# Kernel tuning notes

Hardware: AMD Instinct MI355X
Metric: run time of the kernel (lower is better)

The kernel has to match this reference:

```python
import jax, jax.numpy as jnp
import numpy as np

K = 3
LAST_DIM = 128
IM_H, IM_W = 1024.0, 1536.0
CROP = 2 * K  # tf.image.crop_and_resize crop size [2k, 2k]


def crop_and_resize(image, boxes, box_ids, crop_size):
    """Faithful port of tf.image.crop_and_resize (bilinear, extrapolation=0).
    image: (B,H,W,C); boxes: (N,4) normalized [y1,x1,y2,x2]; box_ids: (N,) int32.
    Returns (N, S, S, C)."""
    H, W = image.shape[1], image.shape[2]
    S = crop_size
    y1, x1, y2, x2 = boxes[:, 0], boxes[:, 1], boxes[:, 2], boxes[:, 3]
    s = jnp.arange(S, dtype=boxes.dtype)
    # sampling coordinates (S > 1 branch of TF)
    ys = y1[:, None] * (H - 1) + s[None, :] * ((y2 - y1)[:, None] * (H - 1) / (S - 1))  # (N,S)
    xs = x1[:, None] * (W - 1) + s[None, :] * ((x2 - x1)[:, None] * (W - 1) / (S - 1))  # (N,S)
    valid_y = (ys >= 0) & (ys <= H - 1)
    valid_x = (xs >= 0) & (xs <= W - 1)
    y0f = jnp.floor(ys)
    x0f = jnp.floor(xs)
    ly = ys - y0f  # bilinear fractions
    lx = xs - x0f
    y0i = jnp.clip(y0f.astype(jnp.int32), 0, H - 1)
    y1i = jnp.clip(y0i + 1, 0, H - 1)
    x0i = jnp.clip(x0f.astype(jnp.int32), 0, W - 1)
    x1i = jnp.clip(x0i + 1, 0, W - 1)
    b = box_ids[:, None, None]

    def g(yi, xi):
        # gather (N,S,S,C) corner values
        return image[b, yi[:, :, None], xi[:, None, :]]

    lx_b = lx[:, None, :, None]
    top = g(y0i, x0i) * (1 - lx_b) + g(y0i, x1i) * lx_b
    bot = g(y1i, x0i) * (1 - lx_b) + g(y1i, x1i) * lx_b
    ly_b = ly[:, :, None, None]
    out = top * (1 - ly_b) + bot * ly_b
    mask = (valid_y[:, :, None] & valid_x[:, None, :]).astype(out.dtype)[..., None]
    return out * mask


def setup_inputs() -> dict:
    key = jax.random.key(0)
    k_feat, k_bid, k_xy, k_wh = jax.random.split(key, 4)
    B, H, W = 4, 64, 96
    N = 2048
    feature_maps = jax.random.normal(k_feat, (B, H, W, K * K * LAST_DIM), dtype=jnp.float32)
    batch_ids = jax.random.randint(k_bid, (N,), 0, B).astype(jnp.float32)
    # top-left corners in image coords, plausible box sizes
    xy = jax.random.uniform(k_xy, (N, 2), dtype=jnp.float32)
    wh = jax.random.uniform(k_wh, (N, 2), dtype=jnp.float32)
    x1 = xy[:, 0] * (0.7 * IM_W)
    y1 = xy[:, 1] * (0.7 * IM_H)
    x2 = x1 + 32.0 + wh[:, 0] * (0.3 * IM_W - 32.0)
    y2 = y1 + 32.0 + wh[:, 1] * (0.3 * IM_H - 32.0)
    rois = jnp.stack([batch_ids, x1, y1, x2, y2], axis=-1)
    return {"feature_maps": feature_maps, "rois": rois}


def reference(feature_maps, rois):
    k = K
    rois = rois.reshape(-1, 5)
    batch_ids = rois[:, 0].astype(jnp.int32)
    norm = jnp.array([IM_W, IM_H, IM_W, IM_H], dtype=rois.dtype)
    bx = rois[:, 1:] / norm                                   # x1,y1,x2,y2 normalized
    boxes = jnp.stack([bx[:, 1], bx[:, 0], bx[:, 3], bx[:, 2]], axis=-1)  # y1,x1,y2,x2
    bin_w = (boxes[:, 3] - boxes[:, 1]) / k
    bin_h = boxes[:, 2] - boxes[:, 0] / k  # faithful bug: missing parens in original
    C = feature_maps.shape[-1] // (k * k)
    acc = 0.0
    for ih in range(k):
        for iw in range(k):
            idx = ih * k + iw
            # faithful bug: fourth coordinate uses bin_h instead of bin_w
            box = jnp.stack([
                boxes[:, 0] + ih * bin_h,
                boxes[:, 1] + iw * bin_w,
                boxes[:, 0] + (ih + 1) * bin_h,
                boxes[:, 1] + (iw + 1) * bin_h,
            ], axis=-1)
            feat = feature_maps[..., idx * C:(idx + 1) * C]
            acc = acc + crop_and_resize(feat, box, batch_ids, CROP)
    sensitive = acc / (k * k)           # (N, 2k, 2k, C)
    out = jnp.mean(sensitive, axis=(1, 2))  # (N, C)
    return out[None]                    # (1, N, C)
```

## Files before the change

kernel.cpp:

```cpp
#include <hip/hip_runtime.h>

constexpr int   CC      = 128;
constexpr int   WSTRIDE = 9 * 128;
constexpr int   HSTRIDE = 96 * WSTRIDE;
constexpr long  BSTRIDE = 64L * HSTRIDE;

__global__ __launch_bounds__(576)
void rroi_pool_kernel(const float* __restrict__ feat,
                      const float* __restrict__ rois,
                      float* __restrict__ out, int N) {
  const int n = blockIdx.x;
  const int wid  = threadIdx.x >> 6;
  const int lane = threadIdx.x & 63;

  __shared__ float partial[9][CC];

  const float r0  = rois[n * 5 + 0];
  const float rx1 = rois[n * 5 + 1];
  const float ry1 = rois[n * 5 + 2];
  const float rx2 = rois[n * 5 + 3];
  const float ry2 = rois[n * 5 + 4];
  const int b = (int)r0;

  const float x1 = rx1 / 1536.0f;
  const float y1 = ry1 / 1024.0f;
  const float x2 = rx2 / 1536.0f;
  const float y2 = ry2 / 1024.0f;

  const float bin_w = (x2 - x1) / 3.0f;
  const float bin_h = y2 - y1 / 3.0f;

  const int ih = wid / 3;
  const int iw = wid - 3 * ih;

  const float by1 = y1 + (float)ih * bin_h;
  const float bx1 = x1 + (float)iw * bin_w;
  const float by2 = y1 + (float)(ih + 1) * bin_h;
  const float bx2 = x1 + (float)(iw + 1) * bin_h;

  const float ystep = ((by2 - by1) * 63.0f) / 5.0f;
  const float xstep = ((bx2 - bx1) * 95.0f) / 5.0f;
  const float ybase = by1 * 63.0f;
  const float xbase = bx1 * 95.0f;

  int   xo0[6], xo1[6];
  float lx[6];
  bool  vx[6];
#pragma unroll
  for (int sx = 0; sx < 6; ++sx) {
    const float xs = xbase + (float)sx * xstep;
    vx[sx] = (xs >= 0.0f) && (xs <= 95.0f);
    const float xf = floorf(xs);
    lx[sx] = xs - xf;
    int xi = (int)xf;
    xi = xi < 0 ? 0 : (xi > 95 ? 95 : xi);
    const int xj = (xi + 1 > 95) ? 95 : xi + 1;
    xo0[sx] = xi * WSTRIDE;
    xo1[sx] = xj * WSTRIDE;
  }

  float acc0 = 0.0f, acc1 = 0.0f;
  const float* fb = feat + (size_t)b * BSTRIDE + wid * CC + 2 * lane;

#pragma unroll
  for (int sy = 0; sy < 6; ++sy) {
    const float ys = ybase + (float)sy * ystep;
    if (!((ys >= 0.0f) && (ys <= 63.0f))) continue;
    const float yf = floorf(ys);
    const float ly = ys - yf;
    int yi = (int)yf;
    yi = yi < 0 ? 0 : (yi > 63 ? 63 : yi);
    const int yj = (yi + 1 > 63) ? 63 : yi + 1;
    const float* row0 = fb + (size_t)yi * HSTRIDE;
    const float* row1 = fb + (size_t)yj * HSTRIDE;
#pragma unroll
    for (int sx = 0; sx < 6; ++sx) {
      if (!vx[sx]) continue;
      const float l = lx[sx];
      const float2 v00 = *(const float2*)(row0 + xo0[sx]);
      const float2 v01 = *(const float2*)(row0 + xo1[sx]);
      const float2 v10 = *(const float2*)(row1 + xo0[sx]);
      const float2 v11 = *(const float2*)(row1 + xo1[sx]);
      const float t0 = v00.x * (1.0f - l) + v01.x * l;
      const float t1 = v00.y * (1.0f - l) + v01.y * l;
      const float u0 = v10.x * (1.0f - l) + v11.x * l;
      const float u1 = v10.y * (1.0f - l) + v11.y * l;
      acc0 += t0 * (1.0f - ly) + u0 * ly;
      acc1 += t1 * (1.0f - ly) + u1 * ly;
    }
  }

  partial[wid][2 * lane]     = acc0;
  partial[wid][2 * lane + 1] = acc1;
  __syncthreads();

  if (threadIdx.x < CC) {
    const float scale = 1.0f / 324.0f;
    float s = 0.0f;
#pragma unroll
    for (int w = 0; w < 9; ++w) s += partial[w][threadIdx.x];
    out[(size_t)n * CC + threadIdx.x] = s * scale;
  }
}

extern "C" void kernel_launch(void* const* d_in, const int* in_sizes, int n_in,
                              void* d_out, int out_size, void* d_ws, size_t ws_size,
                              hipStream_t stream) {
  const float* feat = (const float*)d_in[0];
  const float* rois = (const float*)d_in[1];
  float* out = (float*)d_out;
  const int N = in_sizes[1] / 5;
  rroi_pool_kernel<<<N, 576, 0, stream>>>(feat, rois, out, N);
}
```

Before: 97.99 us.

## Split pooling into per-subbox wave kernel plus separate reduction kernel

```diff
diff --git a/kernel.cpp b/kernel.cpp
--- a/kernel.cpp
+++ b/kernel.cpp
@@ -5,16 +5,10 @@
 constexpr int   HSTRIDE = 96 * WSTRIDE;
 constexpr long  BSTRIDE = 64L * HSTRIDE;
 
-__global__ __launch_bounds__(576)
-void rroi_pool_kernel(const float* __restrict__ feat,
-                      const float* __restrict__ rois,
-                      float* __restrict__ out, int N) {
-  const int n = blockIdx.x;
-  const int wid  = threadIdx.x >> 6;
-  const int lane = threadIdx.x & 63;
-
-  __shared__ float partial[9][CC];
-
+__device__ __forceinline__ void subbox_accum(const float* __restrict__ feat,
+                                             const float* __restrict__ rois,
+                                             int n, int wid, int lane,
+                                             float& acc0, float& acc1) {
   const float r0  = rois[n * 5 + 0];
   const float rx1 = rois[n * 5 + 1];
   const float ry1 = rois[n * 5 + 2];
@@ -59,7 +53,6 @@
     xo1[sx] = xj * WSTRIDE;
   }
 
-  float acc0 = 0.0f, acc1 = 0.0f;
   const float* fb = feat + (size_t)b * BSTRIDE + wid * CC + 2 * lane;
 
 #pragma unroll
@@ -89,17 +82,57 @@
       acc1 += t1 * (1.0f - ly) + u1 * ly;
     }
   }
+}
+
+__global__ __launch_bounds__(64)
+void rroi_partial_kernel(const float* __restrict__ feat,
+                         const float* __restrict__ rois,
+                         float* __restrict__ ws) {
+  const int wid  = blockIdx.x;
+  const int n    = blockIdx.y;
+  const int lane = threadIdx.x;
+
+  float acc0 = 0.0f, acc1 = 0.0f;
+  subbox_accum(feat, rois, n, wid, lane, acc0, acc1);
+
+  float* p = ws + ((size_t)n * 9 + wid) * CC;
+  p[2 * lane]     = acc0;
+  p[2 * lane + 1] = acc1;
+}
+
+__global__ __launch_bounds__(128)
+void rroi_reduce_kernel(const float* __restrict__ ws,
+                        float* __restrict__ out) {
+  const int n = blockIdx.x;
+  const int c = threadIdx.x;
+  const float* p = ws + (size_t)n * 9 * CC + c;
+  float s = 0.0f;
+#pragma unroll
+  for (int w = 0; w < 9; ++w) s += p[w * CC];
+  out[(size_t)n * CC + c] = s * (1.0f / 324.0f);
+}
+
+__global__ __launch_bounds__(576)
+void rroi_pool_kernel(const float* __restrict__ feat,
+                      const float* __restrict__ rois,
+                      float* __restrict__ out, int N) {
+  const int n = blockIdx.x;
+  const int wid  = threadIdx.x >> 6;
+  const int lane = threadIdx.x & 63;
+  __shared__ float partial[9][CC];
+
+  float acc0 = 0.0f, acc1 = 0.0f;
+  subbox_accum(feat, rois, n, wid, lane, acc0, acc1);
 
   partial[wid][2 * lane]     = acc0;
   partial[wid][2 * lane + 1] = acc1;
   __syncthreads();
 
   if (threadIdx.x < CC) {
-    const float scale = 1.0f / 324.0f;
     float s = 0.0f;
 #pragma unroll
     for (int w = 0; w < 9; ++w) s += partial[w][threadIdx.x];
-    out[(size_t)n * CC + threadIdx.x] = s * scale;
+    out[(size_t)n * CC + threadIdx.x] = s * (1.0f / 324.0f);
   }
 }
 
@@ -110,5 +143,14 @@
   const float* rois = (const float*)d_in[1];
   float* out = (float*)d_out;
   const int N = in_sizes[1] / 5;
-  rroi_pool_kernel<<<N, 576, 0, stream>>>(feat, rois, out, N);
+
+  const size_t need = (size_t)N * 9 * CC * sizeof(float);
+  if (ws_size >= need) {
+    float* ws = (float*)d_ws;
+    dim3 grid1(9, N);
+    rroi_partial_kernel<<<grid1, 64, 0, stream>>>(feat, rois, ws);
+    rroi_reduce_kernel<<<N, 128, 0, stream>>>(ws, out);
+  } else {
+    rroi_pool_kernel<<<N, 576, 0, stream>>>(feat, rois, out, N);
+  }
 }
```

After: 95.91 us. 1.02x faster.
